# Kernel optimization log

Hardware: AMD Instinct MI355X
Metric: run time of the kernel (lower is better)

The kernel has to match this reference:

```python
import jax, jax.numpy as jnp
import numpy as np

B_SZ = 8
D_MODEL = 512
D_STATE = 64
N2 = D_STATE // 2  # S4D uses complex-conjugate pairs -> d_state//2 complex modes
L_SEQ = 2048


def setup_inputs() -> dict:
    key = jax.random.key(0)
    ks = jax.random.split(key, 16)
    d = D_MODEL
    scale = 1.0 / np.sqrt(d)
    inp = {
        "x": jax.random.normal(ks[0], (B_SZ, d, L_SEQ), dtype=jnp.float32),
        # q/k/v projections (nn.Linear: weight (out,in), bias (out,))
        "Wq": jax.random.normal(ks[1], (d, d), dtype=jnp.float32) * scale,
        "bq": jax.random.normal(ks[2], (d,), dtype=jnp.float32) * scale,
        "Wk": jax.random.normal(ks[3], (d, d), dtype=jnp.float32) * scale,
        "bk": jax.random.normal(ks[4], (d,), dtype=jnp.float32) * scale,
        "Wv": jax.random.normal(ks[5], (d, d), dtype=jnp.float32) * scale,
        "bv": jax.random.normal(ks[6], (d,), dtype=jnp.float32) * scale,
        # Shift layer params
        "shift_C": jax.random.normal(ks[7], (1, d, D_STATE), dtype=jnp.float32),
        "shift_D": jax.random.normal(ks[8], (d,), dtype=jnp.float32),
        # S4D (diagonal SSM) params
        "log_dt": jax.random.uniform(ks[9], (d,), dtype=jnp.float32,
                                      minval=np.log(1e-3), maxval=np.log(1e-1)),
        "A_real": jnp.log(0.5 * jnp.ones((d, N2), dtype=jnp.float32)),
        "A_imag": jnp.broadcast_to(np.pi * jnp.arange(N2, dtype=jnp.float32), (d, N2)),
        "C_re": jax.random.normal(ks[10], (d, N2), dtype=jnp.float32) * np.sqrt(0.5),
        "C_im": jax.random.normal(ks[11], (d, N2), dtype=jnp.float32) * np.sqrt(0.5),
        "s4_D": jax.random.normal(ks[12], (d,), dtype=jnp.float32),
    }
    return inp


def _linear_chan(x, W, b):
    # x: (B, H, L); Linear applied over channel dim H -> (B, H_out, L)
    return jnp.einsum("bhl,dh->bdl", x, W) + b[:, None]


def _shift(u, C, Dp):
    """Shift SSM: causal conv with kernel = first L taps of C (computed via FFT
    exactly as the torch source does). u: (B, H, L)."""
    L = u.shape[-1]
    n = 2 * L
    H, S = C.shape[1], C.shape[2]
    Bmat = jnp.zeros((H, S), dtype=u.dtype).at[:, 0].set(1.0)
    B_fc = jnp.conj(jnp.fft.rfft(Bmat, n=n, axis=-1))  # (H, L+1)
    C_f = jnp.fft.rfft(C, n=n, axis=-1)                # (1, H, L+1)
    kernel = jnp.fft.irfft(B_fc * C_f, n=n, axis=-1)[..., :L]  # (1, H, L)
    kernel_f = jnp.fft.rfft(kernel, n=n, axis=-1)      # (1, H, L+1)
    u_f = jnp.fft.rfft(u, n=n, axis=-1)                # (B, H, L+1)
    y = jnp.fft.irfft(u_f * kernel_f, n=n, axis=-1)[..., :L]
    return y + u * Dp[:, None]


def _s4d(u, log_dt, A_real, A_imag, C_re, C_im, Dp):
    """Standard S4D forward: ZOH-discretized diagonal SSM kernel + FFT conv.
    u: (B, H, L)."""
    L = u.shape[-1]
    n = 2 * L
    dt = jnp.exp(log_dt)[:, None]                  # (H, 1)
    A = -jnp.exp(A_real) + 1j * A_imag             # (H, N2)
    dtA = A * dt                                   # (H, N2)
    C = (C_re + 1j * C_im) * (jnp.exp(dtA) - 1.0) / A
    vand = jnp.exp(dtA[:, :, None] * jnp.arange(L))  # (H, N2, L)
    K = 2.0 * jnp.einsum("hn,hnl->hl", C, vand).real  # (H, L)
    y = jnp.fft.irfft(jnp.fft.rfft(u, n=n, axis=-1) * jnp.fft.rfft(K, n=n, axis=-1),
                      n=n, axis=-1)[..., :L]
    return y + u * Dp[:, None]


def reference(x, Wq, bq, Wk, bk, Wv, bv, shift_C, shift_D,
              log_dt, A_real, A_imag, C_re, C_im, s4_D):
    q = _linear_chan(x, Wq, bq)
    k = _linear_chan(x, Wk, bk)
    v = _linear_chan(x, Wv, bv)
    shift_out = _shift(k, shift_C, shift_D)
    s4d_out = _s4d(v * shift_out, log_dt, A_real, A_imag, C_re, C_im, s4_D)
    return q * s4d_out
```

## Files before the change

### kernel.cpp

```cpp
#include <hip/hip_runtime.h>
#include <cstdint>


#define DMODEL 512
#define LSEQ 2048

typedef _Float16 half_t;
typedef __attribute__((ext_vector_type(4))) _Float16 half4v;
typedef __attribute__((ext_vector_type(8))) _Float16 half8v;
typedef __attribute__((ext_vector_type(4))) float floatx4;

#define SW(R, c) ((R) * 64 + ((((c) >> 3) ^ ((R) & 7)) << 3) + ((c) & 7))

__device__ __forceinline__ void gload_lds16(const half_t* g, half_t* l) {
  __builtin_amdgcn_global_load_lds(
      (const __attribute__((address_space(1))) uint32_t*)g,
      (__attribute__((address_space(3))) uint32_t*)l, 16, 0, 0);
}

__global__ __launch_bounds__(256) void convert_w(
    const float* __restrict__ Wq, const float* __restrict__ Wk,
    const float* __restrict__ Wv, half_t* __restrict__ W16) {
  int i = blockIdx.x * 256 + threadIdx.x;
  const float* src = (i < 262144) ? Wq : ((i < 524288) ? Wk : Wv);
  int j = i & 262143;
  W16[i] = (half_t)src[j];
}

__global__ __launch_bounds__(256) void transpose_x(
    const float* __restrict__ x, half_t* __restrict__ xT) {
  __shared__ float tile[32][33];
  int b = blockIdx.z;
  int d0 = blockIdx.y * 32;
  int l0 = blockIdx.x * 32;
  int tx = threadIdx.x, ty = threadIdx.y;
  const float* xp = x + (size_t)b * DMODEL * LSEQ;
#pragma unroll
  for (int k = 0; k < 4; k++)
    tile[ty + 8 * k][tx] = xp[(size_t)(d0 + ty + 8 * k) * LSEQ + l0 + tx];
  __syncthreads();
  half_t* op = xT + (size_t)b * LSEQ * DMODEL;
#pragma unroll
  for (int k = 0; k < 4; k++)
    op[(size_t)(l0 + ty + 8 * k) * DMODEL + d0 + tx] = (half_t)tile[tx][ty + 8 * k];
}

__global__ __launch_bounds__(256) void s4d_tables(
    const float* __restrict__ log_dt, const float* __restrict__ A_real,
    const float* __restrict__ A_imag, const float* __restrict__ C_re,
    const float* __restrict__ C_im, const float* __restrict__ shC,
    half_t* __restrict__ Vt, half_t* __restrict__ Et, half_t* __restrict__ Tt,
    half_t* __restrict__ T1t, half_t* __restrict__ T2t,
    float* __restrict__ wt2) {
  __shared__ float aL[32], bL[32], wrL[32], wiL[32], crL[32], ciL[32];
  __shared__ float Kt[64], tapl[64];
  int h = blockIdx.x;
  int tid = threadIdx.x;
  if (tid < 64) { Kt[tid] = 0.f; tapl[tid] = shC[h * 64 + tid]; }
  if (tid < 32) {
    int n = tid, hn = h * 32 + n;
    float dt = expf(log_dt[h]);
    float Ar = -expf(A_real[hn]), Ai = A_imag[hn];
    float a = dt * Ar, b = dt * Ai;
    float ea = expf(a);
    float wr = ea * cosf(b), wi = ea * sinf(b);
    float Am2 = Ar * Ar + Ai * Ai;
    float zr = wr - 1.0f, zi = wi;
    float qr = (zr * Ar + zi * Ai) / Am2;
    float qi = (zi * Ar - zr * Ai) / Am2;
    aL[n] = a; bL[n] = b; wrL[n] = wr; wiL[n] = wi;
    crL[n] = C_re[hn] * qr - C_im[hn] * qi;
    ciL[n] = C_re[hn] * qi + C_im[hn] * qr;
    float e64 = expf(64.0f * a);
    wt2[h * 64 + 2 * n]     = e64 * cosf(64.0f * b);
    wt2[h * 64 + 2 * n + 1] = e64 * sinf(64.0f * b);
  }
  __syncthreads();
  size_t base = (size_t)h * 4096;
  {
    int r = tid >> 2;
    int nb = (tid & 3) * 8;
    float ksum = 0.f;
#pragma unroll
    for (int i = 0; i < 8; i++) {
      int n = nb + i;
      float a = aL[n], b = bL[n];
      float cr = crL[n], ci = ciL[n];
      float er = expf(a * (float)r);
      float w0r = er * cosf(b * (float)r), w0i = er * sinf(b * (float)r);
      ksum += 2.f * (cr * w0r - ci * w0i);
      float wr = wrL[n], wi = wiL[n];
      float w1r = w0r * wr - w0i * wi, w1i = w0r * wi + w0i * wr;
      Et[base + SW(r, 2 * n)]     = (half_t)(2.f * (cr * w1r - ci * w1i));
      Et[base + SW(r, 2 * n + 1)] = (half_t)(-2.f * (cr * w1i + ci * w1r));
      Vt[base + SW(2 * n, 63 - r)]     = (half_t)w0r;
      Vt[base + SW(2 * n + 1, 63 - r)] = (half_t)w0i;
    }
    atomicAdd(&Kt[r], ksum);
  }
  __syncthreads();
#pragma unroll
  for (int e = 0; e < 16; e++) {
    int idx = e * 256 + tid;
    int r = idx >> 6, t = idx & 63;
    int d = r - t;
    size_t a = base + SW(r, t);
    Tt[a]  = (d >= 0) ? (half_t)Kt[d] : (half_t)0.f;
    T1t[a] = (d >= 0) ? (half_t)tapl[d] : (half_t)0.f;
    T2t[a] = (d < 0) ? (half_t)tapl[64 + d] : (half_t)0.f;
  }
}

__global__ __launch_bounds__(256) void gemm_qkv(
    const half_t* __restrict__ xT, const half_t* __restrict__ Wstk,
    const float* __restrict__ bq, const float* __restrict__ bk,
    const float* __restrict__ bv, half_t* __restrict__ outq,
    half_t* __restrict__ outk, half_t* __restrict__ outv) {
  __shared__ half_t As[2][128 * 32];
  __shared__ half_t Bs[2][128 * 32];
  int flat = blockIdx.x;
  int swz = (flat & 7) * 192 + (flat >> 3);
  int nt = swz / 12, mt = swz - nt * 12;
  int n0 = nt * 128, m0 = mt * 128;
  int tid = threadIdx.x;
  int lane = tid & 63, wid = tid >> 6;
  int wr = wid >> 1, wc = wid & 1;
  int lrow = lane & 15, lg = lane >> 4;
  int r_in = lane >> 2, s_in = lane & 3;

  floatx4 acc[4][4];
#pragma unroll
  for (int i = 0; i < 4; i++)
#pragma unroll
    for (int j = 0; j < 4; j++) acc[i][j] = (floatx4){0.f, 0.f, 0.f, 0.f};

  auto STAGE = [&](int buf, int kk) {
#pragma unroll
    for (int i = 0; i < 2; i++) {
      int c = wid * 2 + i;
      int row = c * 16 + r_in;
      int ss = s_in ^ ((row >> 1) & 3);
      gload_lds16(Wstk + (size_t)(m0 + row) * 512 + kk + ss * 8,
                  &As[buf][c * 512]);
      gload_lds16(xT + (size_t)(n0 + row) * 512 + kk + ss * 8,
                  &Bs[buf][c * 512]);
    }
  };

  STAGE(0, 0);
  __syncthreads();
  int cur = 0;
  for (int t = 0; t < 16; t++) {
    if (t < 15) STAGE(cur ^ 1, (t + 1) * 32);
    half8v af[4], bf[4];
#pragma unroll
    for (int i = 0; i < 4; i++) {
      int r = wr * 64 + i * 16 + lrow;
      af[i] = *(const half8v*)(&As[cur][r * 32 + (lg ^ ((r >> 1) & 3)) * 8]);
    }
#pragma unroll
    for (int j = 0; j < 4; j++) {
      int r = wc * 64 + j * 16 + lrow;
      bf[j] = *(const half8v*)(&Bs[cur][r * 32 + (lg ^ ((r >> 1) & 3)) * 8]);
    }
#pragma unroll
    for (int i = 0; i < 4; i++)
#pragma unroll
      for (int j = 0; j < 4; j++)
        acc[i][j] = __builtin_amdgcn_mfma_f32_16x16x32_f16(af[i], bf[j],
                                                           acc[i][j], 0, 0, 0);
    __syncthreads();
    cur ^= 1;
  }

  int z = m0 >> 9;
  const float* bias = (z == 0) ? bq : ((z == 1) ? bk : bv);
  half_t* outp = (z == 0) ? outq : ((z == 1) ? outk : outv);
#pragma unroll
  for (int i = 0; i < 4; i++) {
    int d = (m0 + wr * 64 + i * 16 + 4 * lg) & 511;
#pragma unroll
    for (int j = 0; j < 4; j++) {
      int n = n0 + wc * 64 + j * 16 + lrow;
      int b = n >> 11, l = n & 2047;
#pragma unroll
      for (int reg = 0; reg < 4; reg++) {
        float val = acc[i][j][reg] + bias[d + reg];
        size_t bhbase = ((size_t)(b * 512 + d + reg)) * 2048;
        if (z == 0) {
          outp[bhbase + l] = (half_t)val;
        } else {
          int jj = l >> 6, c = l & 63;
          outp[bhbase + SW(jj, c)] = (half_t)val;
        }
      }
    }
  }
}

__global__ __launch_bounds__(256) void s4d_main(
    const half_t* __restrict__ kimg, const half_t* __restrict__ vimg,
    const half_t* __restrict__ T1t, const half_t* __restrict__ T2t,
    const half_t* __restrict__ Vt, const half_t* __restrict__ Et,
    const half_t* __restrict__ Tt, const float* __restrict__ wt2,
    const float* __restrict__ shD, const float* __restrict__ s4D,
    const half_t* __restrict__ qbuf, float* __restrict__ outp) {
  __shared__ half_t kl[33 * 64];
  __shared__ half_t vg[32 * 64];
  __shared__ half_t uh[32 * 64];
  __shared__ half_t tab0[64 * 64];
  __shared__ half_t tab1[64 * 64];
  __shared__ half_t tab2[64 * 64];
  __shared__ float SG[32 * 66];
  int bh = blockIdx.x;
  int h = bh & 511;
  int tid = threadIdx.x;
  int lane = tid & 63, wid = tid >> 6;
  int lrow = lane & 15, lg = lane >> 4;
  int mi = wid & 1;
  int ri0 = wid >> 1;

  {
    const half_t* kp = kimg + (size_t)bh * 2048;
    const half_t* vp = vimg + (size_t)bh * 2048;
    size_t tb = (size_t)h * 4096;
    gload_lds16(kp + wid * 512 + lane * 8, kl + 64 + wid * 512);
    gload_lds16(vp + wid * 512 + lane * 8, vg + wid * 512);
#pragma unroll
    for (int i = 0; i < 2; i++) {
      int c = wid * 2 + i;
      gload_lds16(T1t + tb + c * 512 + lane * 8, tab0 + c * 512);
      gload_lds16(T2t + tb + c * 512 + lane * 8, tab1 + c * 512);
      gload_lds16(Vt + tb + c * 512 + lane * 8, tab2 + c * 512);
    }
  }
  if (tid < 8) {
    half8v zz = {(_Float16)0, (_Float16)0, (_Float16)0, (_Float16)0,
                 (_Float16)0, (_Float16)0, (_Float16)0, (_Float16)0};
    *(half8v*)(kl + tid * 8) = zz;
  }
  float sDsh = shD[h];
  float sD4 = s4D[h];
  __syncthreads();

#define LDF(base, r, ks, key) \
  (*(const half8v*)((base) + (r) * 64 + (((ks) * 4 + lg) ^ (key)) * 8))

  floatx4 acc[2];
  acc[0] = (floatx4){0.f, 0.f, 0.f, 0.f};
  acc[1] = (floatx4){0.f, 0.f, 0.f, 0.f};
  {
    int jA = mi * 16 + lrow;
    int key1 = lrow & 7, key2 = (lrow + 7) & 7;
#pragma unroll
    for (int ks = 0; ks < 2; ks++) {
      half8v a1 = LDF(kl, 1 + jA, ks, key1);
      half8v a2 = LDF(kl, jA, ks, key2);
#pragma unroll
      for (int tt = 0; tt < 2; tt++) {
        int rb = (ri0 + tt * 2) * 16 + lrow;
        half8v b1 = LDF(tab0, rb, ks, lrow & 7);
        half8v b2 = LDF(tab1, rb, ks, lrow & 7);
        acc[tt] = __builtin_amdgcn_mfma_f32_16x16x32_f16(a1, b1, acc[tt], 0, 0, 0);
        acc[tt] = __builtin_amdgcn_mfma_f32_16x16x32_f16(a2, b2, acc[tt], 0, 0, 0);
      }
    }
  }
#pragma unroll
  for (int tt = 0; tt < 2; tt++) {
#pragma unroll
    for (int reg = 0; reg < 4; reg++) {
      int j = mi * 16 + 4 * lg + reg;
      int r = (ri0 + tt * 2) * 16 + lrow;
      int cph = (((r >> 3) ^ (j & 7)) << 3) + (r & 7);
      float kvv = (float)kl[(1 + j) * 64 + cph];
      float vvv = (float)vg[j * 64 + cph];
      uh[j * 64 + cph] = (half_t)(vvv * (acc[tt][reg] + sDsh * kvv));
    }
  }
  __syncthreads();

  {
    size_t tb = (size_t)h * 4096;
#pragma unroll
    for (int i = 0; i < 2; i++) {
      int c = wid * 2 + i;
      gload_lds16(Et + tb + c * 512 + lane * 8, tab0 + c * 512);
      gload_lds16(Tt + tb + c * 512 + lane * 8, tab1 + c * 512);
    }
  }

  acc[0] = (floatx4){0.f, 0.f, 0.f, 0.f};
  acc[1] = (floatx4){0.f, 0.f, 0.f, 0.f};
#pragma unroll
  for (int ks = 0; ks < 2; ks++) {
    half8v a = LDF(uh, mi * 16 + lrow, ks, lrow & 7);
#pragma unroll
    for (int tt = 0; tt < 2; tt++) {
      int rb = (ri0 + tt * 2) * 16 + lrow;
      half8v b = LDF(tab2, rb, ks, lrow & 7);
      acc[tt] = __builtin_amdgcn_mfma_f32_16x16x32_f16(a, b, acc[tt], 0, 0, 0);
    }
  }
#pragma unroll
  for (int tt = 0; tt < 2; tt++) {
    int ri = ri0 + tt * 2;
#pragma unroll
    for (int reg = 0; reg < 4; reg++) {
      int j = mi * 16 + 4 * lg + reg;
      SG[j * 66 + ri * 16 + lrow] = acc[tt][reg];
    }
  }
  __syncthreads();

  if (tid < 32) {
    int n = tid;
    float wTr = wt2[h * 64 + 2 * n], wTi = wt2[h * 64 + 2 * n + 1];
    float gr = 0.f, gi = 0.f;
    for (int j = 0; j < 32; j++) {
      float tr = SG[j * 66 + 2 * n], ti = SG[j * 66 + 2 * n + 1];
      SG[j * 66 + 2 * n] = gr; SG[j * 66 + 2 * n + 1] = gi;
      float nr = wTr * gr - wTi * gi + tr;
      gi = wTr * gi + wTi * gr + ti;
      gr = nr;
    }
  }
  __syncthreads();

  {
    int j = tid >> 3, s = tid & 7;
    half8v g;
#pragma unroll
    for (int i = 0; i < 8; i++) g[i] = (half_t)SG[j * 66 + s * 8 + i];
    *(half8v*)(vg + j * 64 + (s ^ (j & 7)) * 8) = g;
  }
  __syncthreads();

  acc[0] = (floatx4){0.f, 0.f, 0.f, 0.f};
  acc[1] = (floatx4){0.f, 0.f, 0.f, 0.f};
#pragma unroll
  for (int ks = 0; ks < 2; ks++) {
    half8v ag = LDF(vg, mi * 16 + lrow, ks, lrow & 7);
    half8v au = LDF(uh, mi * 16 + lrow, ks, lrow & 7);
#pragma unroll
    for (int tt = 0; tt < 2; tt++) {
      int rb = (ri0 + tt * 2) * 16 + lrow;
      half8v be = LDF(tab0, rb, ks, lrow & 7);
      half8v bt = LDF(tab1, rb, ks, lrow & 7);
      acc[tt] = __builtin_amdgcn_mfma_f32_16x16x32_f16(ag, be, acc[tt], 0, 0, 0);
      acc[tt] = __builtin_amdgcn_mfma_f32_16x16x32_f16(au, bt, acc[tt], 0, 0, 0);
    }
  }
  const half_t* qp = qbuf + (size_t)bh * 2048;
  float* op = outp + (size_t)bh * 2048;
#pragma unroll
  for (int tt = 0; tt < 2; tt++) {
#pragma unroll
    for (int reg = 0; reg < 4; reg++) {
      int j = mi * 16 + 4 * lg + reg;
      int r = (ri0 + tt * 2) * 16 + lrow;
      int cph = (((r >> 3) ^ (j & 7)) << 3) + (r & 7);
      float y = acc[tt][reg] + sD4 * (float)uh[j * 64 + cph];
      int l = j * 64 + r;
      op[l] = (float)qp[l] * y;
    }
  }
#undef LDF
}

extern "C" void kernel_launch(void* const* d_in, const int* in_sizes, int n_in,
                              void* d_out, int out_size, void* d_ws, size_t ws_size,
                              hipStream_t stream) {
  const float* x      = (const float*)d_in[0];
  const float* Wq     = (const float*)d_in[1];
  const float* bq     = (const float*)d_in[2];
  const float* Wk     = (const float*)d_in[3];
  const float* bk     = (const float*)d_in[4];
  const float* Wv     = (const float*)d_in[5];
  const float* bv     = (const float*)d_in[6];
  const float* shC    = (const float*)d_in[7];
  const float* shD    = (const float*)d_in[8];
  const float* log_dt = (const float*)d_in[9];
  const float* A_real = (const float*)d_in[10];
  const float* A_imag = (const float*)d_in[11];
  const float* C_re   = (const float*)d_in[12];
  const float* C_im   = (const float*)d_in[13];
  const float* s4D    = (const float*)d_in[14];
  float* out = (float*)d_out;
  half_t* wsh = (half_t*)d_ws;

  half_t* qbuf = wsh;
  half_t* kbuf = wsh + 8388608;
  half_t* vbuf = wsh + 16777216;
  half_t* xT16 = wsh + 25165824;
  half_t* W16  = wsh + 33554432;
  half_t* Vt   = wsh + 34340864;
  half_t* Et   = wsh + 36438016;
  half_t* Tt   = wsh + 38535168;
  half_t* T1t  = wsh + 40632320;
  half_t* T2t  = wsh + 42729472;
  float*  wt2  = (float*)(wsh + 44826624);

  convert_w<<<3072, 256, 0, stream>>>(Wq, Wk, Wv, W16);
  transpose_x<<<dim3(64, 16, 8), dim3(32, 8), 0, stream>>>(x, xT16);
  s4d_tables<<<512, 256, 0, stream>>>(log_dt, A_real, A_imag, C_re, C_im, shC,
                                      Vt, Et, Tt, T1t, T2t, wt2);
  gemm_qkv<<<dim3(1536), 256, 0, stream>>>(xT16, W16, bq, bk, bv,
                                           qbuf, kbuf, vbuf);
  s4d_main<<<4096, 256, 0, stream>>>(kbuf, vbuf, T1t, T2t, Vt, Et, Tt,
                                     wt2, shD, s4D, qbuf, out);
}
```

Baseline: 96.53 us.

## Enlarge QKV GEMM tiles to 256x256 with triple-buffered LDS pipeline

The QKV projection GEMM now uses 256x256 output tiles with 512-thread blocks (8 waves, each computing 128x64), instead of 128x128 tiles with 256 threads. A three-stage LDS ring buffer in dynamic shared memory prefetches two k-steps ahead and splits each stage load into halves that are interleaved with the MFMA phases. It also raises wave priority around the MFMAs and uses explicit vmcnt waits with raw barriers. The aim is more data reuse per tile and better overlap of global loads with matrix math. The cost is more registers per thread and 96KB of LDS, which may limit occupancy, and the grid drops to 384 blocks, which may leave some CUs idle.

```diff
diff --git a/kernel.cpp b/kernel.cpp
--- a/kernel.cpp
+++ b/kernel.cpp
@@ -111,77 +111,105 @@
   }
 }
 
-__global__ __launch_bounds__(256) void gemm_qkv(
+__global__ __launch_bounds__(512, 2) void gemm_qkv(
     const half_t* __restrict__ xT, const half_t* __restrict__ Wstk,
     const float* __restrict__ bq, const float* __restrict__ bk,
     const float* __restrict__ bv, half_t* __restrict__ outq,
     half_t* __restrict__ outk, half_t* __restrict__ outv) {
-  __shared__ half_t As[2][128 * 32];
-  __shared__ half_t Bs[2][128 * 32];
+  extern __shared__ half_t smem[];
+  half_t* ldsA = smem;
+  half_t* ldsB = smem + 24576;
   int flat = blockIdx.x;
-  int swz = (flat & 7) * 192 + (flat >> 3);
-  int nt = swz / 12, mt = swz - nt * 12;
-  int n0 = nt * 128, m0 = mt * 128;
+  int swz = (flat & 7) * 48 + (flat >> 3);
+  int nt = swz / 6, mt = swz - nt * 6;
+  int n0 = nt * 256, m0 = mt * 256;
   int tid = threadIdx.x;
   int lane = tid & 63, wid = tid >> 6;
-  int wr = wid >> 1, wc = wid & 1;
+  int wm = wid >> 2, wn = wid & 3;
   int lrow = lane & 15, lg = lane >> 4;
-  int r_in = lane >> 2, s_in = lane & 3;
-
-  floatx4 acc[4][4];
-#pragma unroll
-  for (int i = 0; i < 4; i++)
+  int r_in = tid >> 2;
+  int s_in = (tid & 3) ^ ((r_in >> 1) & 3);
+
+  const half_t* gA = Wstk + (size_t)(m0 + r_in) * 512 + s_in * 8;
+  const half_t* gB = xT + (size_t)(n0 + r_in) * 512 + s_in * 8;
+  int dst = tid * 8;
+
+  floatx4 acc[8][4];
+#pragma unroll
+  for (int i = 0; i < 8; i++)
 #pragma unroll
     for (int j = 0; j < 4; j++) acc[i][j] = (floatx4){0.f, 0.f, 0.f, 0.f};
 
-  auto STAGE = [&](int buf, int kk) {
-#pragma unroll
-    for (int i = 0; i < 2; i++) {
-      int c = wid * 2 + i;
-      int row = c * 16 + r_in;
-      int ss = s_in ^ ((row >> 1) & 3);
-      gload_lds16(Wstk + (size_t)(m0 + row) * 512 + kk + ss * 8,
-                  &As[buf][c * 512]);
-      gload_lds16(xT + (size_t)(n0 + row) * 512 + kk + ss * 8,
-                  &Bs[buf][c * 512]);
-    }
-  };
-
-  STAGE(0, 0);
-  __syncthreads();
-  int cur = 0;
+#define STAGE(buf, kt, ih)                                                   \
+  do {                                                                       \
+    gload_lds16(gA + (size_t)(ih)*65536 + (kt)*32,                           \
+                ldsA + (buf)*8192 + (ih)*4096 + dst);                        \
+    gload_lds16(gB + (size_t)(ih)*65536 + (kt)*32,                           \
+                ldsB + (buf)*8192 + (ih)*4096 + dst);                        \
+  } while (0)
+
+  STAGE(0, 0, 0); STAGE(0, 0, 1);
+  STAGE(1, 1, 0); STAGE(1, 1, 1);
+  asm volatile("s_waitcnt vmcnt(4)" ::: "memory");
+  __builtin_amdgcn_s_barrier();
+
+  int cur = 0, stb = 2;
   for (int t = 0; t < 16; t++) {
-    if (t < 15) STAGE(cur ^ 1, (t + 1) * 32);
+    const half_t* Ac = ldsA + cur * 8192;
+    const half_t* Bc = ldsB + cur * 8192;
     half8v af[4], bf[4];
 #pragma unroll
     for (int i = 0; i < 4; i++) {
-      int r = wr * 64 + i * 16 + lrow;
-      af[i] = *(const half8v*)(&As[cur][r * 32 + (lg ^ ((r >> 1) & 3)) * 8]);
+      int ra = wm * 128 + i * 16 + lrow;
+      af[i] = *(const half8v*)(Ac + ra * 32 + ((lg ^ ((ra >> 1) & 3)) << 3));
     }
 #pragma unroll
     for (int j = 0; j < 4; j++) {
-      int r = wc * 64 + j * 16 + lrow;
-      bf[j] = *(const half8v*)(&Bs[cur][r * 32 + (lg ^ ((r >> 1) & 3)) * 8]);
-    }
+      int rb = wn * 64 + j * 16 + lrow;
+      bf[j] = *(const half8v*)(Bc + rb * 32 + ((lg ^ ((rb >> 1) & 3)) << 3));
+    }
+    if (t < 14) STAGE(stb, t + 2, 0);
+    __builtin_amdgcn_s_setprio(1);
 #pragma unroll
     for (int i = 0; i < 4; i++)
 #pragma unroll
       for (int j = 0; j < 4; j++)
         acc[i][j] = __builtin_amdgcn_mfma_f32_16x16x32_f16(af[i], bf[j],
                                                            acc[i][j], 0, 0, 0);
-    __syncthreads();
-    cur ^= 1;
-  }
+    __builtin_amdgcn_s_setprio(0);
+    __builtin_amdgcn_s_barrier();
+#pragma unroll
+    for (int i = 0; i < 4; i++) {
+      int ra = wm * 128 + 64 + i * 16 + lrow;
+      af[i] = *(const half8v*)(Ac + ra * 32 + ((lg ^ ((ra >> 1) & 3)) << 3));
+    }
+    if (t < 14) STAGE(stb, t + 2, 1);
+    __builtin_amdgcn_s_setprio(1);
+#pragma unroll
+    for (int i = 0; i < 4; i++)
+#pragma unroll
+      for (int j = 0; j < 4; j++)
+        acc[4 + i][j] = __builtin_amdgcn_mfma_f32_16x16x32_f16(af[i], bf[j],
+                                                               acc[4 + i][j],
+                                                               0, 0, 0);
+    __builtin_amdgcn_s_setprio(0);
+    if (t < 14) asm volatile("s_waitcnt vmcnt(4)" ::: "memory");
+    else        asm volatile("s_waitcnt vmcnt(0)" ::: "memory");
+    __builtin_amdgcn_s_barrier();
+    cur = (cur == 2) ? 0 : cur + 1;
+    stb = (stb == 2) ? 0 : stb + 1;
+  }
+#undef STAGE
 
   int z = m0 >> 9;
   const float* bias = (z == 0) ? bq : ((z == 1) ? bk : bv);
   half_t* outp = (z == 0) ? outq : ((z == 1) ? outk : outv);
 #pragma unroll
-  for (int i = 0; i < 4; i++) {
-    int d = (m0 + wr * 64 + i * 16 + 4 * lg) & 511;
+  for (int i = 0; i < 8; i++) {
+    int d = (m0 + wm * 128 + i * 16 + 4 * lg) & 511;
 #pragma unroll
     for (int j = 0; j < 4; j++) {
-      int n = n0 + wc * 64 + j * 16 + lrow;
+      int n = n0 + wn * 64 + j * 16 + lrow;
       int b = n >> 11, l = n & 2047;
 #pragma unroll
       for (int reg = 0; reg < 4; reg++) {
@@ -401,12 +429,15 @@
   half_t* T2t  = wsh + 42729472;
   float*  wt2  = (float*)(wsh + 44826624);
 
+  hipFuncSetAttribute((const void*)gemm_qkv,
+                      hipFuncAttributeMaxDynamicSharedMemorySize, 98304);
+
   convert_w<<<3072, 256, 0, stream>>>(Wq, Wk, Wv, W16);
   transpose_x<<<dim3(64, 16, 8), dim3(32, 8), 0, stream>>>(x, xT16);
   s4d_tables<<<512, 256, 0, stream>>>(log_dt, A_real, A_imag, C_re, C_im, shC,
                                       Vt, Et, Tt, T1t, T2t, wt2);
-  gemm_qkv<<<dim3(1536), 256, 0, stream>>>(xT16, W16, bq, bk, bv,
-                                           qbuf, kbuf, vbuf);
+  gemm_qkv<<<dim3(384), 512, 98304, stream>>>(xT16, W16, bq, bk, bv,
+                                              qbuf, kbuf, vbuf);
   s4d_main<<<4096, 256, 0, stream>>>(kbuf, vbuf, T1t, T2t, Vt, Et, Tt,
                                      wt2, shD, s4D, qbuf, out);
 }
```

Result: no change. 96.76 us (+0.2%).

## Vectorize transpose, restage GEMM with K=64 tiles and LDS-staged coalesced epilogues

Applied to the files above, without the earlier changes.

The x transpose now uses 64x64 tiles with float4 loads and 8-wide half stores. The QKV GEMM drops double buffering in favour of single-buffered 64-wide K tiles with an XOR swizzle, so it does half as many barrier rounds. Its epilogue goes through LDS so that output rows are written as 16-byte vectors. The s4d_main epilogue also stages results in shared memory (SG) so the q multiply and the final stores are coalesced and vectorized. Without double buffering the GEMM loses load/compute overlap, and each kernel gains extra barriers.

```diff
diff --git a/kernel.cpp b/kernel.cpp
--- a/kernel.cpp
+++ b/kernel.cpp
@@ -29,20 +29,29 @@
 
 __global__ __launch_bounds__(256) void transpose_x(
     const float* __restrict__ x, half_t* __restrict__ xT) {
-  __shared__ float tile[32][33];
+  __shared__ float tile[64][68];
   int b = blockIdx.z;
-  int d0 = blockIdx.y * 32;
-  int l0 = blockIdx.x * 32;
-  int tx = threadIdx.x, ty = threadIdx.y;
-  const float* xp = x + (size_t)b * DMODEL * LSEQ;
-#pragma unroll
-  for (int k = 0; k < 4; k++)
-    tile[ty + 8 * k][tx] = xp[(size_t)(d0 + ty + 8 * k) * LSEQ + l0 + tx];
-  __syncthreads();
-  half_t* op = xT + (size_t)b * LSEQ * DMODEL;
-#pragma unroll
-  for (int k = 0; k < 4; k++)
-    op[(size_t)(l0 + ty + 8 * k) * DMODEL + d0 + tx] = (half_t)tile[tx][ty + 8 * k];
+  int d0 = blockIdx.y * 64;
+  int l0 = blockIdx.x * 64;
+  int t = threadIdx.x;
+  int dy = t >> 4, lx = t & 15;
+  const float* xp = x + ((size_t)(b * 512 + d0)) * 2048 + l0;
+#pragma unroll
+  for (int rr = 0; rr < 4; rr++) {
+    float4 v = *(const float4*)(xp + (size_t)(rr * 16 + dy) * 2048 + lx * 4);
+    *(float4*)&tile[rr * 16 + dy][lx * 4] = v;
+  }
+  __syncthreads();
+  half_t* op = xT + ((size_t)(b * 2048 + l0)) * 512 + d0;
+  int lr = t >> 2, c4 = t & 3;
+#pragma unroll
+  for (int cc = 0; cc < 2; cc++) {
+    int ch = cc * 4 + c4;
+    half8v hv;
+#pragma unroll
+    for (int e = 0; e < 8; e++) hv[e] = (half_t)tile[ch * 8 + e][lr];
+    *(half8v*)(op + (size_t)lr * 512 + ch * 8) = hv;
+  }
 }
 
 __global__ __launch_bounds__(256) void s4d_tables(
@@ -116,8 +125,9 @@
     const float* __restrict__ bq, const float* __restrict__ bk,
     const float* __restrict__ bv, half_t* __restrict__ outq,
     half_t* __restrict__ outk, half_t* __restrict__ outv) {
-  __shared__ half_t As[2][128 * 32];
-  __shared__ half_t Bs[2][128 * 32];
+  __shared__ half_t smem[16384];
+  half_t* As = smem;
+  half_t* Bs = smem + 8192;
   int flat = blockIdx.x;
   int swz = (flat & 7) * 192 + (flat >> 3);
   int nt = swz / 12, mt = swz - nt * 12;
@@ -126,7 +136,8 @@
   int lane = tid & 63, wid = tid >> 6;
   int wr = wid >> 1, wc = wid & 1;
   int lrow = lane & 15, lg = lane >> 4;
-  int r_in = lane >> 2, s_in = lane & 3;
+  int rsub = lane >> 3, ssub = lane & 7;
+  int gslot = ssub ^ rsub;
 
   floatx4 acc[4][4];
 #pragma unroll
@@ -134,65 +145,74 @@
 #pragma unroll
     for (int j = 0; j < 4; j++) acc[i][j] = (floatx4){0.f, 0.f, 0.f, 0.f};
 
-  auto STAGE = [&](int buf, int kk) {
-#pragma unroll
-    for (int i = 0; i < 2; i++) {
-      int c = wid * 2 + i;
-      int row = c * 16 + r_in;
-      int ss = s_in ^ ((row >> 1) & 3);
-      gload_lds16(Wstk + (size_t)(m0 + row) * 512 + kk + ss * 8,
-                  &As[buf][c * 512]);
-      gload_lds16(xT + (size_t)(n0 + row) * 512 + kk + ss * 8,
-                  &Bs[buf][c * 512]);
-    }
-  };
-
-  STAGE(0, 0);
-  __syncthreads();
-  int cur = 0;
-  for (int t = 0; t < 16; t++) {
-    if (t < 15) STAGE(cur ^ 1, (t + 1) * 32);
-    half8v af[4], bf[4];
+  const half_t* gA = Wstk + (size_t)(m0 + wid * 32 + rsub) * 512 + gslot * 8;
+  const half_t* gB = xT + (size_t)(n0 + wid * 32 + rsub) * 512 + gslot * 8;
+
+  for (int kk = 0; kk < 512; kk += 64) {
 #pragma unroll
     for (int i = 0; i < 4; i++) {
-      int r = wr * 64 + i * 16 + lrow;
-      af[i] = *(const half8v*)(&As[cur][r * 32 + (lg ^ ((r >> 1) & 3)) * 8]);
-    }
-#pragma unroll
-    for (int j = 0; j < 4; j++) {
-      int r = wc * 64 + j * 16 + lrow;
-      bf[j] = *(const half8v*)(&Bs[cur][r * 32 + (lg ^ ((r >> 1) & 3)) * 8]);
-    }
-#pragma unroll
-    for (int i = 0; i < 4; i++)
-#pragma unroll
-      for (int j = 0; j < 4; j++)
-        acc[i][j] = __builtin_amdgcn_mfma_f32_16x16x32_f16(af[i], bf[j],
-                                                           acc[i][j], 0, 0, 0);
+      int c = wid * 4 + i;
+      gload_lds16(gA + (size_t)i * 8 * 512 + kk, As + c * 512);
+      gload_lds16(gB + (size_t)i * 8 * 512 + kk, Bs + c * 512);
+    }
     __syncthreads();
-    cur ^= 1;
+#pragma unroll
+    for (int h = 0; h < 2; h++) {
+      half8v af[4], bf[4];
+#pragma unroll
+      for (int i = 0; i < 4; i++) {
+        int r = wr * 64 + i * 16 + lrow;
+        af[i] = *(const half8v*)(As + r * 64 + ((h * 4 + lg) ^ (r & 7)) * 8);
+      }
+#pragma unroll
+      for (int j = 0; j < 4; j++) {
+        int r = wc * 64 + j * 16 + lrow;
+        bf[j] = *(const half8v*)(Bs + r * 64 + ((h * 4 + lg) ^ (r & 7)) * 8);
+      }
+#pragma unroll
+      for (int i = 0; i < 4; i++)
+#pragma unroll
+        for (int j = 0; j < 4; j++)
+          acc[i][j] = __builtin_amdgcn_mfma_f32_16x16x32_f16(af[i], bf[j],
+                                                             acc[i][j], 0, 0, 0);
+    }
+    __syncthreads();
   }
 
   int z = m0 >> 9;
   const float* bias = (z == 0) ? bq : ((z == 1) ? bk : bv);
-  half_t* outp = (z == 0) ? outq : ((z == 1) ? outk : outv);
+  half_t* smemC = smem;
 #pragma unroll
   for (int i = 0; i < 4; i++) {
-    int d = (m0 + wr * 64 + i * 16 + 4 * lg) & 511;
+    int dl = wr * 64 + i * 16 + 4 * lg;
+    float4 b4 = *(const float4*)&bias[(m0 + dl) & 511];
 #pragma unroll
     for (int j = 0; j < 4; j++) {
-      int n = n0 + wc * 64 + j * 16 + lrow;
-      int b = n >> 11, l = n & 2047;
+      int ll = wc * 64 + j * 16 + lrow;
 #pragma unroll
       for (int reg = 0; reg < 4; reg++) {
-        float val = acc[i][j][reg] + bias[d + reg];
-        size_t bhbase = ((size_t)(b * 512 + d + reg)) * 2048;
-        if (z == 0) {
-          outp[bhbase + l] = (half_t)val;
-        } else {
-          int jj = l >> 6, c = l & 63;
-          outp[bhbase + SW(jj, c)] = (half_t)val;
-        }
+        int d = dl + reg;
+        float val = acc[i][j][reg] + ((const float*)&b4)[reg];
+        smemC[d * 128 + (((ll >> 3) ^ (d & 15)) << 3) + (ll & 7)] = (half_t)val;
+      }
+    }
+  }
+  __syncthreads();
+  {
+    int t4 = tid >> 4, ch = tid & 15;
+    int b = n0 >> 11, l0 = n0 & 2047;
+    half_t* outp = (z == 0) ? outq : ((z == 1) ? outk : outv);
+#pragma unroll
+    for (int rep = 0; rep < 8; rep++) {
+      int d = rep * 16 + t4;
+      half8v v = *(const half8v*)(smemC + d * 128 + ((ch ^ (d & 15)) << 3));
+      size_t rowb = ((size_t)(b * 512 + ((m0 + d) & 511))) * 2048;
+      if (z == 0) {
+        *(half8v*)(outp + rowb + l0 + ch * 8) = v;
+      } else {
+        int j = (l0 >> 6) + (ch >> 3);
+        int s = ch & 7;
+        *(half8v*)(outp + rowb + j * 64 + ((s ^ (j & 7)) << 3)) = v;
       }
     }
   }
@@ -351,8 +371,6 @@
       acc[tt] = __builtin_amdgcn_mfma_f32_16x16x32_f16(au, bt, acc[tt], 0, 0, 0);
     }
   }
-  const half_t* qp = qbuf + (size_t)bh * 2048;
-  float* op = outp + (size_t)bh * 2048;
 #pragma unroll
   for (int tt = 0; tt < 2; tt++) {
 #pragma unroll
@@ -360,10 +378,26 @@
       int j = mi * 16 + 4 * lg + reg;
       int r = (ri0 + tt * 2) * 16 + lrow;
       int cph = (((r >> 3) ^ (j & 7)) << 3) + (r & 7);
-      float y = acc[tt][reg] + sD4 * (float)uh[j * 64 + cph];
-      int l = j * 64 + r;
-      op[l] = (float)qp[l] * y;
-    }
+      SG[j * 64 + r] = acc[tt][reg] + sD4 * (float)uh[j * 64 + cph];
+    }
+  }
+  __syncthreads();
+
+  {
+    const half_t* qp = qbuf + (size_t)bh * 2048;
+    float* op = outp + (size_t)bh * 2048;
+    half8v qv = *(const half8v*)(qp + tid * 8);
+    float4 o0, o1;
+    o0.x = (float)qv[0] * SG[tid * 8 + 0];
+    o0.y = (float)qv[1] * SG[tid * 8 + 1];
+    o0.z = (float)qv[2] * SG[tid * 8 + 2];
+    o0.w = (float)qv[3] * SG[tid * 8 + 3];
+    o1.x = (float)qv[4] * SG[tid * 8 + 4];
+    o1.y = (float)qv[5] * SG[tid * 8 + 5];
+    o1.z = (float)qv[6] * SG[tid * 8 + 6];
+    o1.w = (float)qv[7] * SG[tid * 8 + 7];
+    *(float4*)(op + tid * 8) = o0;
+    *(float4*)(op + tid * 8 + 4) = o1;
   }
 #undef LDF
 }
@@ -402,7 +436,7 @@
   float*  wt2  = (float*)(wsh + 44826624);
 
   convert_w<<<3072, 256, 0, stream>>>(Wq, Wk, Wv, W16);
-  transpose_x<<<dim3(64, 16, 8), dim3(32, 8), 0, stream>>>(x, xT16);
+  transpose_x<<<dim3(32, 8, 8), 256, 0, stream>>>(x, xT16);
   s4d_tables<<<512, 256, 0, stream>>>(log_dt, A_real, A_imag, C_re, C_im, shC,
                                       Vt, Et, Tt, T1t, T2t, wt2);
   gemm_qkv<<<dim3(1536), 256, 0, stream>>>(xT16, W16, bq, bk, bv,
```

Result: no change. 95.85 us (-0.7%).
